# Performance work log

Measured on AMD Instinct MI355X. Metric: run time of the kernel, lower is better.

## Reference

```python
import jax, jax.numpy as jnp
import numpy as np

H = 81  # number_of_cells
EPS = 1e-5

def setup_inputs() -> dict:
    key = jax.random.key(0)
    ks = jax.random.split(key, 16)
    B, T, F = 512, 1024, 128
    s_ih = 1.0 / np.sqrt(H)
    inp = {
        'x':     jax.random.normal(ks[0], (B, 1, T, F), dtype=jnp.float32),
        'W_ih':  jax.random.uniform(ks[1], (3 * H, F), jnp.float32, -s_ih, s_ih),
        'W_hh':  jax.random.uniform(ks[2], (3 * H, H), jnp.float32, -s_ih, s_ih),
        'b_ih':  jax.random.uniform(ks[3], (3 * H,), jnp.float32, -s_ih, s_ih),
        'b_hh':  jax.random.uniform(ks[4], (3 * H,), jnp.float32, -s_ih, s_ih),
        'fc_w':  jax.random.uniform(ks[5], (8, H), jnp.float32, -s_ih, s_ih),
        'fc_b':  jax.random.uniform(ks[6], (8,), jnp.float32, -s_ih, s_ih),
        'g1':    jnp.ones((8,), jnp.float32),
        'beta1': jnp.zeros((8,), jnp.float32),
        'fc1_w': jax.random.uniform(ks[7], (4, 8), jnp.float32, -np.sqrt(1/8), np.sqrt(1/8)),
        'fc1_b': jax.random.uniform(ks[8], (4,), jnp.float32, -np.sqrt(1/8), np.sqrt(1/8)),
        'g2':    jnp.ones((4,), jnp.float32),
        'beta2': jnp.zeros((4,), jnp.float32),
        'fc2_w': jax.random.uniform(ks[9], (1, 4), jnp.float32, -0.5, 0.5),
        'fc2_b': jax.random.uniform(ks[10], (1,), jnp.float32, -0.5, 0.5),
    }
    return inp

def _batchnorm(x, g, b):
    mu = jnp.mean(x, axis=0)
    var = jnp.var(x, axis=0)  # biased, as torch uses for normalization
    return (x - mu) * jax.lax.rsqrt(var + EPS) * g + b

def _gru_last_hidden(x, W_ih, W_hh, b_ih, b_hh):
    # x: [B, T, F]; PyTorch gate order: r, z, n
    B = x.shape[0]
    xg = jnp.einsum('btf,gf->tbg', x, W_ih) + b_ih  # [T, B, 3H]
    h0 = jnp.zeros((B, H), x.dtype)

    def step(h, xg_t):
        hg = h @ W_hh.T + b_hh
        xr, xz, xn = jnp.split(xg_t, 3, axis=-1)
        hr, hz, hn = jnp.split(hg, 3, axis=-1)
        r = jax.nn.sigmoid(xr + hr)
        z = jax.nn.sigmoid(xz + hz)
        n = jnp.tanh(xn + r * hn)
        h_new = (1.0 - z) * n + z * h
        return h_new, None

    h_last, _ = jax.lax.scan(step, h0, xg)
    return h_last  # [B, H]

def reference(x, W_ih, W_hh, b_ih, b_hh, fc_w, fc_b, g1, beta1, fc1_w, fc1_b, g2, beta2, fc2_w, fc2_b):
    B = x.shape[0]
    xs = x.reshape(B, x.shape[2], x.shape[3])  # view(B, T, F)
    h = _gru_last_hidden(xs, W_ih, W_hh, b_ih, b_hh)
    out = h @ fc_w.T + fc_b            # GRU0.fc on last timestep -> [B, 8]
    out = jax.nn.silu(out)
    out = _batchnorm(out, g1, beta1)
    out = jax.nn.silu(out @ fc1_w.T + fc1_b)
    out = _batchnorm(out, g2, beta2)
    out = out @ fc2_w.T + fc2_b        # [B, 1]
    return out
```

## Files before the change

### kernel.cpp

```cpp
#include <hip/hip_runtime.h>

#define B_  512
#define T_  1024
#define F_  128
#define H_  81
#define G3  243
#define GPX 244

typedef unsigned short u16;
typedef __attribute__((ext_vector_type(8))) short bf16x8;
typedef __attribute__((ext_vector_type(4))) float f32x4;
typedef __attribute__((ext_vector_type(2))) float f32x2;

__device__ __forceinline__ float bf2f(u16 u) {
    union { unsigned int i; float f; } v; v.i = ((unsigned int)u) << 16; return v.f;
}
__device__ __forceinline__ u16 f2bf(float f) {
    union { float f; unsigned int i; } v; v.f = f;
    unsigned int i = v.i;
    return (u16)((i + 0x7fffu + ((i >> 16) & 1u)) >> 16);
}
__device__ __forceinline__ float rcp_(float x) { return __builtin_amdgcn_rcpf(x); }
__device__ __forceinline__ float sigmoidf_(float x) { return rcp_(1.f + __expf(-x)); }
__device__ __forceinline__ float tanhf_(float x) {
    return fmaf(-2.f, rcp_(__expf(2.f * x) + 1.f), 1.f);
}
__device__ __forceinline__ void barrier_nodrain() {
    asm volatile("s_waitcnt lgkmcnt(0)\n\ts_barrier" ::: "memory");
}

__global__ void wsplit_kernel(const float* __restrict__ W,
                              u16* __restrict__ hi, u16* __restrict__ lo)
{
    const int i = blockIdx.x * 256 + threadIdx.x;
    if (i < G3 * F_) {
        const float v = W[i];
        const u16 h = f2bf(v);
        hi[i] = h;
        lo[i] = f2bf(v - bf2f(h));
    }
}

__global__ __launch_bounds__(256, 2) void xg_gemm(const float* __restrict__ x,
                                                  const u16* __restrict__ Whi,
                                                  const u16* __restrict__ Wlo,
                                                  const float* __restrict__ b_ih,
                                                  float* __restrict__ xg)
{
    __shared__ __align__(16) u16 ws_hi[G3][64];
    __shared__ __align__(16) u16 ws_lo[G3][64];

    const int tid  = threadIdx.x;
    const int wave = tid >> 6, lane = tid & 63;
    const int l15  = lane & 15, q = lane >> 4;
    const int b    = blockIdx.x & 511;
    const int t0   = (blockIdx.x >> 9) << 7;

    f32x4 acc[2][16];
#pragma unroll
    for (int mt = 0; mt < 2; ++mt)
#pragma unroll
        for (int gt = 0; gt < 16; ++gt) acc[mt][gt] = (f32x4){0.f, 0.f, 0.f, 0.f};

    for (int half = 0; half < 2; ++half) {
        if (half) __syncthreads();
#pragma unroll
        for (int it = 0; it < 16; ++it) {
            const int i = it * 256 + tid;
            if (i < 2 * G3 * 8) {
                const bool lo = (i >= G3 * 8);
                const int j = lo ? (i - G3 * 8) : i;
                const int g = j >> 3, c = j & 7;
                const uint4 v = *(const uint4*)((lo ? Wlo : Whi)
                                                + (size_t)g * F_ + half * 64 + c * 8);
                *(uint4*)&((lo ? ws_lo : ws_hi)[g][((c + g) & 7) * 8]) = v;
            }
        }
        __syncthreads();

#pragma unroll
        for (int kcl = 0; kcl < 2; ++kcl) {
            bf16x8 aHi[2], aLo[2];
#pragma unroll
            for (int mt = 0; mt < 2; ++mt) {
                const float* xr = x + ((size_t)b * T_ + t0 + (wave * 2 + mt) * 16 + l15) * F_
                                  + half * 64 + kcl * 32 + q * 8;
                float xv[8];
                *(float4*)&xv[0] = *(const float4*)(xr);
                *(float4*)&xv[4] = *(const float4*)(xr + 4);
#pragma unroll
                for (int j = 0; j < 8; ++j) {
                    const u16 h = f2bf(xv[j]);
                    aHi[mt][j] = (short)h;
                    aLo[mt][j] = (short)f2bf(xv[j] - bf2f(h));
                }
            }
#pragma unroll
            for (int gt = 0; gt < 16; ++gt) {
                const int gr  = gt * 16 + l15;
                const int grc = (gr < G3) ? gr : (G3 - 1);
                const int sl  = ((kcl * 4 + q + grc) & 7) * 8;
                const bf16x8 bHi = *(const bf16x8*)&ws_hi[grc][sl];
                const bf16x8 bLo = *(const bf16x8*)&ws_lo[grc][sl];
#pragma unroll
                for (int mt = 0; mt < 2; ++mt) {
                    acc[mt][gt] = __builtin_amdgcn_mfma_f32_16x16x32_bf16(aHi[mt], bHi, acc[mt][gt], 0, 0, 0);
                    acc[mt][gt] = __builtin_amdgcn_mfma_f32_16x16x32_bf16(aHi[mt], bLo, acc[mt][gt], 0, 0, 0);
                    acc[mt][gt] = __builtin_amdgcn_mfma_f32_16x16x32_bf16(aLo[mt], bHi, acc[mt][gt], 0, 0, 0);
                }
            }
        }
    }
#pragma unroll
    for (int gt = 0; gt < 16; ++gt) {
        const int g = gt * 16 + l15;
        if (g < G3) {
            const float bias = b_ih[g];
#pragma unroll
            for (int mt = 0; mt < 2; ++mt) {
                const int trow = t0 + (wave * 2 + mt) * 16 + q * 4;
#pragma unroll
                for (int c = 0; c < 4; ++c)
                    xg[((size_t)b * T_ + trow + c) * GPX + g] = acc[mt][gt][c] + bias;
            }
        }
    }
}

__global__ __launch_bounds__(256, 1) void gru_kernel(const float* __restrict__ xg,
                                                     const float* __restrict__ W_hh,
                                                     const float* __restrict__ b_hh,
                                                     float* __restrict__ h_out)
{
    __shared__ __align__(16) float h_s[2][88];
    __shared__ float part[2][3][244];
    __shared__ float xn_s[2][84];

    const int tid = threadIdx.x;
    const int b0 = blockIdx.x * 2, b1 = b0 + 1;
    const bool act = tid < G3;
    const int p   = (tid >= 162) ? 2 : ((tid >= 81) ? 1 : 0);
    const int j   = act ? (tid - p * 81) : 0;
    const int k0  = p * 28;

    f32x2 w2[3][14];
#pragma unroll
    for (int i = 0; i < 3; ++i) {
        const float* wr = W_hh + (size_t)(j + 81 * i) * H_ + k0;
#pragma unroll
        for (int c = 0; c < 14; ++c) {
            const float e0 = (act && (k0 + 2 * c)     < H_) ? wr[2 * c]     : 0.f;
            const float e1 = (act && (k0 + 2 * c + 1) < H_) ? wr[2 * c + 1] : 0.f;
            w2[i][c] = (f32x2){e0, e1};
        }
    }
#pragma unroll
    for (int i = 0; i < 3; ++i)
#pragma unroll
        for (int c = 0; c < 14; ++c)
            asm volatile("" : "+v"(w2[i][c]));

    const int gq = (tid < H_) ? 0 : ((tid >= 128 && tid < 128 + H_) ? 1 : -1);
    const int gi = (gq == 1) ? (tid - 128) : tid;
    const float br = (gq >= 0) ? b_hh[gi]          : 0.f;
    const float bz = (gq >= 0) ? b_hh[H_ + gi]     : 0.f;
    const float bn = (gq >= 0) ? b_hh[2 * H_ + gi] : 0.f;
    float hreg = 0.f;

    if (tid < 176) ((float*)h_s)[tid] = 0.f;
    __syncthreads();

    const float* xp0 = xg + (size_t)b0 * T_ * GPX + (act ? tid : 0);
    const float* xp1 = xg + (size_t)b1 * T_ * GPX + (act ? tid : 0);
    float xf0[4], xf1[4];
#pragma unroll
    for (int u = 0; u < 4; ++u) {
        xf0[u] = xp0[(size_t)u * GPX];
        xf1[u] = xp1[(size_t)u * GPX];
    }

    for (int t4 = 0; t4 < T_; t4 += 4) {
#pragma unroll
        for (int u = 0; u < 4; ++u) {
            const float xv0 = xf0[u], xv1 = xf1[u];
            f32x2 aA0[3], aB0[3], aA1[3], aB1[3];
#pragma unroll
            for (int i = 0; i < 3; ++i) {
                aA0[i] = (f32x2){0.f, 0.f}; aB0[i] = (f32x2){0.f, 0.f};
                aA1[i] = (f32x2){0.f, 0.f}; aB1[i] = (f32x2){0.f, 0.f};
            }
#pragma unroll
            for (int c = 0; c < 7; ++c) {
                const float4 h40 = ((const float4*)h_s[0])[p * 7 + c];
                const float4 h41 = ((const float4*)h_s[1])[p * 7 + c];
                const f32x2 lo0 = {h40.x, h40.y}, hi0 = {h40.z, h40.w};
                const f32x2 lo1 = {h41.x, h41.y}, hi1 = {h41.z, h41.w};
#pragma unroll
                for (int i = 0; i < 3; ++i) {
                    aA0[i] = __builtin_elementwise_fma(w2[i][2 * c],     lo0, aA0[i]);
                    aB0[i] = __builtin_elementwise_fma(w2[i][2 * c + 1], hi0, aB0[i]);
                    aA1[i] = __builtin_elementwise_fma(w2[i][2 * c],     lo1, aA1[i]);
                    aB1[i] = __builtin_elementwise_fma(w2[i][2 * c + 1], hi1, aB1[i]);
                }
            }
            const f32x2 t00 = aA0[0] + aB0[0], t01 = aA0[1] + aB0[1], t02 = aA0[2] + aB0[2];
            const f32x2 t10 = aA1[0] + aB1[0], t11 = aA1[1] + aB1[1], t12 = aA1[2] + aB1[2];
            float s00 = t00.x + t00.y, s01 = t01.x + t01.y, s02 = t02.x + t02.y;
            float s10 = t10.x + t10.y, s11 = t11.x + t11.y, s12 = t12.x + t12.y;
            s00 += (p == 0) ? xv0 : 0.f;
            s01 += (p == 1) ? xv0 : 0.f;
            s10 += (p == 0) ? xv1 : 0.f;
            s11 += (p == 1) ? xv1 : 0.f;
            if (act) {
                if (p == 2) { xn_s[0][j] = xv0; xn_s[1][j] = xv1; }
                part[0][p][j]       = s00;
                part[0][p][j + 81]  = s01;
                part[0][p][j + 162] = s02;
                part[1][p][j]       = s10;
                part[1][p][j + 81]  = s11;
                part[1][p][j + 162] = s12;
            }
            barrier_nodrain();
            if (gq >= 0) {
                const float prer = part[gq][0][gi]       + part[gq][1][gi]       + part[gq][2][gi]       + br;
                const float prez = part[gq][0][gi + 81]  + part[gq][1][gi + 81]  + part[gq][2][gi + 81]  + bz;
                const float hn   = part[gq][0][gi + 162] + part[gq][1][gi + 162] + part[gq][2][gi + 162] + bn;
                const float rr = sigmoidf_(prer);
                const float zz = sigmoidf_(prez);
                const float nn = tanhf_(fmaf(rr, hn, xn_s[gq][gi]));
                hreg = nn + zz * (hreg - nn);
                h_s[gq][gi] = hreg;
            }
            barrier_nodrain();
            const int tn = (t4 + u + 4 < T_) ? (t4 + u + 4) : (T_ - 1);
            xf0[u] = xp0[(size_t)tn * GPX];
            xf1[u] = xp1[(size_t)tn * GPX];
        }
    }

    if (gq == 0)      h_out[(size_t)b0 * H_ + gi] = hreg;
    else if (gq == 1) h_out[(size_t)b1 * H_ + gi] = hreg;
}

__device__ __forceinline__ float block_sum(float v, float* red, int tid) {
#pragma unroll
    for (int off = 32; off; off >>= 1) v += __shfl_down(v, off, 64);
    const int wid = tid >> 6;
    if ((tid & 63) == 0) red[wid] = v;
    __syncthreads();
    if (tid == 0) {
        float s = 0.f;
#pragma unroll
        for (int i = 0; i < 8; ++i) s += red[i];
        red[8] = s;
    }
    __syncthreads();
    const float s = red[8];
    __syncthreads();
    return s;
}

__global__ __launch_bounds__(512) void head_kernel(const float* __restrict__ h_out,
                                                   const float* __restrict__ fc_w,
                                                   const float* __restrict__ fc_b,
                                                   const float* __restrict__ g1,
                                                   const float* __restrict__ beta1,
                                                   const float* __restrict__ fc1_w,
                                                   const float* __restrict__ fc1_b,
                                                   const float* __restrict__ g2,
                                                   const float* __restrict__ beta2,
                                                   const float* __restrict__ fc2_w,
                                                   const float* __restrict__ fc2_b,
                                                   float* __restrict__ out)
{
    __shared__ float red[9];
    const int tid = threadIdx.x;
    const float inv = 1.f / 512.f;

    float hv[H_];
    const float* hp = h_out + (size_t)tid * H_;
#pragma unroll
    for (int c = 0; c < H_; ++c) hv[c] = hp[c];

    float o[8];
#pragma unroll
    for (int j = 0; j < 8; ++j) {
        float s = fc_b[j];
        for (int c = 0; c < H_; ++c) s += hv[c] * fc_w[j * H_ + c];
        o[j] = s * sigmoidf_(s);
    }
#pragma unroll
    for (int j = 0; j < 8; ++j) {
        const float mu = block_sum(o[j], red, tid) * inv;
        const float m2 = block_sum(o[j] * o[j], red, tid) * inv;
        o[j] = (o[j] - mu) * rsqrtf(m2 - mu * mu + 1e-5f) * g1[j] + beta1[j];
    }
    float p[4];
#pragma unroll
    for (int i = 0; i < 4; ++i) {
        float s = fc1_b[i];
#pragma unroll
        for (int j = 0; j < 8; ++j) s += o[j] * fc1_w[i * 8 + j];
        p[i] = s * sigmoidf_(s);
    }
#pragma unroll
    for (int i = 0; i < 4; ++i) {
        const float mu = block_sum(p[i], red, tid) * inv;
        const float m2 = block_sum(p[i] * p[i], red, tid) * inv;
        p[i] = (p[i] - mu) * rsqrtf(m2 - mu * mu + 1e-5f) * g2[i] + beta2[i];
    }
    float res = fc2_b[0];
#pragma unroll
    for (int i = 0; i < 4; ++i) res += p[i] * fc2_w[i];
    out[tid] = res;
}

extern "C" void kernel_launch(void* const* d_in, const int* in_sizes, int n_in,
                              void* d_out, int out_size, void* d_ws, size_t ws_size,
                              hipStream_t stream)
{
    const float* x     = (const float*)d_in[0];
    const float* W_ih  = (const float*)d_in[1];
    const float* W_hh  = (const float*)d_in[2];
    const float* b_ih  = (const float*)d_in[3];
    const float* b_hh  = (const float*)d_in[4];

    float* xg    = (float*)d_ws;
    float* h_out = xg + (size_t)B_ * T_ * GPX;
    u16*   Whi   = (u16*)(h_out + B_ * H_);
    u16*   Wlo   = Whi + G3 * F_;

    wsplit_kernel<<<dim3((G3 * F_ + 255) / 256), dim3(256), 0, stream>>>(W_ih, Whi, Wlo);
    xg_gemm<<<dim3(512 * 8), dim3(256), 0, stream>>>(x, Whi, Wlo, b_ih, xg);
    gru_kernel<<<dim3(B_ / 2), dim3(256), 0, stream>>>(xg, W_hh, b_hh, h_out);
    head_kernel<<<dim3(1), dim3(512), 0, stream>>>(h_out,
        (const float*)d_in[5], (const float*)d_in[6], (const float*)d_in[7],
        (const float*)d_in[8], (const float*)d_in[9], (const float*)d_in[10],
        (const float*)d_in[11], (const float*)d_in[12], (const float*)d_in[13],
        (const float*)d_in[14], (float*)d_out);
}
```

Baseline: 1.153 ms.

## Stagger two batch rows so one's dot product overlaps the other's gate update

```diff
diff --git a/kernel.cpp b/kernel.cpp
--- a/kernel.cpp
+++ b/kernel.cpp
@@ -179,62 +179,67 @@
         xf1[u] = xp1[(size_t)u * GPX];
     }
 
+    auto DOT = [&](int bb, float xv) {
+        f32x2 aA0 = {0.f, 0.f}, aA1 = {0.f, 0.f}, aA2 = {0.f, 0.f};
+        f32x2 aB0 = {0.f, 0.f}, aB1 = {0.f, 0.f}, aB2 = {0.f, 0.f};
+#pragma unroll
+        for (int c = 0; c < 7; ++c) {
+            const float4 h4 = ((const float4*)h_s[bb])[p * 7 + c];
+            const f32x2 lo = {h4.x, h4.y}, hi = {h4.z, h4.w};
+            aA0 = __builtin_elementwise_fma(w2[0][2 * c],     lo, aA0);
+            aB0 = __builtin_elementwise_fma(w2[0][2 * c + 1], hi, aB0);
+            aA1 = __builtin_elementwise_fma(w2[1][2 * c],     lo, aA1);
+            aB1 = __builtin_elementwise_fma(w2[1][2 * c + 1], hi, aB1);
+            aA2 = __builtin_elementwise_fma(w2[2][2 * c],     lo, aA2);
+            aB2 = __builtin_elementwise_fma(w2[2][2 * c + 1], hi, aB2);
+        }
+        const f32x2 t0 = aA0 + aB0, t1 = aA1 + aB1, t2 = aA2 + aB2;
+        float s0 = t0.x + t0.y + ((p == 0) ? xv : 0.f);
+        float s1 = t1.x + t1.y + ((p == 1) ? xv : 0.f);
+        const float s2 = t2.x + t2.y;
+        if (act) {
+            if (p == 2) xn_s[bb][j] = xv;
+            part[bb][p][j]       = s0;
+            part[bb][p][j + 81]  = s1;
+            part[bb][p][j + 162] = s2;
+        }
+    };
+    auto GATE = [&](int bb) {
+        if (gq == bb) {
+            const float prer = part[bb][0][gi]       + part[bb][1][gi]       + part[bb][2][gi]       + br;
+            const float prez = part[bb][0][gi + 81]  + part[bb][1][gi + 81]  + part[bb][2][gi + 81]  + bz;
+            const float hn   = part[bb][0][gi + 162] + part[bb][1][gi + 162] + part[bb][2][gi + 162] + bn;
+            const float rr = sigmoidf_(prer);
+            const float zz = sigmoidf_(prez);
+            const float nn = tanhf_(fmaf(rr, hn, xn_s[bb][gi]));
+            hreg = nn + zz * (hreg - nn);
+            h_s[bb][gi] = hreg;
+        }
+    };
+
+    DOT(0, xf0[0]);
+    barrier_nodrain();
+    xf0[0] = xp0[(size_t)4 * GPX];
+
     for (int t4 = 0; t4 < T_; t4 += 4) {
 #pragma unroll
         for (int u = 0; u < 4; ++u) {
-            const float xv0 = xf0[u], xv1 = xf1[u];
-            f32x2 aA0[3], aB0[3], aA1[3], aB1[3];
-#pragma unroll
-            for (int i = 0; i < 3; ++i) {
-                aA0[i] = (f32x2){0.f, 0.f}; aB0[i] = (f32x2){0.f, 0.f};
-                aA1[i] = (f32x2){0.f, 0.f}; aB1[i] = (f32x2){0.f, 0.f};
-            }
-#pragma unroll
-            for (int c = 0; c < 7; ++c) {
-                const float4 h40 = ((const float4*)h_s[0])[p * 7 + c];
-                const float4 h41 = ((const float4*)h_s[1])[p * 7 + c];
-                const f32x2 lo0 = {h40.x, h40.y}, hi0 = {h40.z, h40.w};
-                const f32x2 lo1 = {h41.x, h41.y}, hi1 = {h41.z, h41.w};
-#pragma unroll
-                for (int i = 0; i < 3; ++i) {
-                    aA0[i] = __builtin_elementwise_fma(w2[i][2 * c],     lo0, aA0[i]);
-                    aB0[i] = __builtin_elementwise_fma(w2[i][2 * c + 1], hi0, aB0[i]);
-                    aA1[i] = __builtin_elementwise_fma(w2[i][2 * c],     lo1, aA1[i]);
-                    aB1[i] = __builtin_elementwise_fma(w2[i][2 * c + 1], hi1, aB1[i]);
-                }
-            }
-            const f32x2 t00 = aA0[0] + aB0[0], t01 = aA0[1] + aB0[1], t02 = aA0[2] + aB0[2];
-            const f32x2 t10 = aA1[0] + aB1[0], t11 = aA1[1] + aB1[1], t12 = aA1[2] + aB1[2];
-            float s00 = t00.x + t00.y, s01 = t01.x + t01.y, s02 = t02.x + t02.y;
-            float s10 = t10.x + t10.y, s11 = t11.x + t11.y, s12 = t12.x + t12.y;
-            s00 += (p == 0) ? xv0 : 0.f;
-            s01 += (p == 1) ? xv0 : 0.f;
-            s10 += (p == 0) ? xv1 : 0.f;
-            s11 += (p == 1) ? xv1 : 0.f;
-            if (act) {
-                if (p == 2) { xn_s[0][j] = xv0; xn_s[1][j] = xv1; }
-                part[0][p][j]       = s00;
-                part[0][p][j + 81]  = s01;
-                part[0][p][j + 162] = s02;
-                part[1][p][j]       = s10;
-                part[1][p][j + 81]  = s11;
-                part[1][p][j + 162] = s12;
-            }
+            const int t = t4 + u;
+            DOT(1, xf1[u]);
+            GATE(0);
             barrier_nodrain();
-            if (gq >= 0) {
-                const float prer = part[gq][0][gi]       + part[gq][1][gi]       + part[gq][2][gi]       + br;
-                const float prez = part[gq][0][gi + 81]  + part[gq][1][gi + 81]  + part[gq][2][gi + 81]  + bz;
-                const float hn   = part[gq][0][gi + 162] + part[gq][1][gi + 162] + part[gq][2][gi + 162] + bn;
-                const float rr = sigmoidf_(prer);
-                const float zz = sigmoidf_(prez);
-                const float nn = tanhf_(fmaf(rr, hn, xn_s[gq][gi]));
-                hreg = nn + zz * (hreg - nn);
-                h_s[gq][gi] = hreg;
-            }
+            {
+                const int tn = (t + 4 < T_) ? (t + 4) : (T_ - 1);
+                xf1[u] = xp1[(size_t)tn * GPX];
+            }
+            const int un = (u + 1) & 3;
+            DOT(0, xf0[un]);
+            GATE(1);
             barrier_nodrain();
-            const int tn = (t4 + u + 4 < T_) ? (t4 + u + 4) : (T_ - 1);
-            xf0[u] = xp0[(size_t)tn * GPX];
-            xf1[u] = xp1[(size_t)tn * GPX];
+            {
+                const int tn = (t + 5 < T_) ? (t + 5) : (T_ - 1);
+                xf0[un] = xp0[(size_t)tn * GPX];
+            }
         }
     }
 
```

Result: slower. 1.363 ms (+18.2%).
